# Performance work log

Measured on AMD Instinct MI355X. Metric: run time of the kernel, lower is better.

The kernel has to match this reference:

```python
import jax, jax.numpy as jnp
import numpy as np

N, NCLS, D = 512, 100000, 128
SCALE, MARGIN = 64.0, 0.5
EPS_BN = 1e-5
EPS_NORM = 1e-12


def _init_conv(key, shape):
    # Kaiming-ish init for conv weights (OIHW)
    fan_in = float(np.prod(shape[1:]))
    return jax.random.normal(key, shape, jnp.float32) * np.float32(np.sqrt(2.0 / fan_in))


def setup_inputs() -> dict:
    key = jax.random.key(0)
    ks = jax.random.split(key, 8)
    return {
        "x": jax.random.normal(ks[0], (N, 1, 112, 112), jnp.float32),
        "gt": jax.random.randint(ks[1], (N,), 0, NCLS, dtype=jnp.int32),
        "w1": _init_conv(ks[2], (16, 1, 4, 4)),  "b1": jnp.zeros(16),  "g1": jnp.ones(16),  "be1": jnp.zeros(16),
        "w2": _init_conv(ks[3], (32, 16, 4, 4)), "b2": jnp.zeros(32),  "g2": jnp.ones(32),  "be2": jnp.zeros(32),
        "w3": _init_conv(ks[4], (64, 32, 3, 3)), "b3": jnp.zeros(64),  "g3": jnp.ones(64),  "be3": jnp.zeros(64),
        "w4": _init_conv(ks[5], (128, 64, 3, 3)),"b4": jnp.zeros(128), "g4": jnp.ones(128), "be4": jnp.zeros(128),
        # xavier-uniform ArcFace weight (out_size, in_size)
        "arc_w": jax.random.uniform(ks[6], (NCLS, D), jnp.float32, -1.0, 1.0) * np.float32(np.sqrt(6.0 / (NCLS + D))),
    }


def _conv_bn_relu(x, w, b, g, be, stride, pad):
    y = jax.lax.conv_general_dilated(
        x, w, (stride, stride), [(pad, pad), (pad, pad)],
        dimension_numbers=("NCHW", "OIHW", "NCHW"))
    y = y + b[None, :, None, None]
    # BatchNorm in training mode: batch statistics, biased variance
    mu = y.mean((0, 2, 3), keepdims=True)
    var = ((y - mu) ** 2).mean((0, 2, 3), keepdims=True)
    yn = (y - mu) * jax.lax.rsqrt(var + EPS_BN)
    return jax.nn.relu(yn * g[None, :, None, None] + be[None, :, None, None])


def _l2norm(v):
    return v / jnp.maximum(jnp.linalg.norm(v, axis=1, keepdims=True), EPS_NORM)


def reference(x, gt, w1, b1, g1, be1, w2, b2, g2, be2, w3, b3, g3, be3,
              w4, b4, g4, be4, arc_w):
    h = _conv_bn_relu(x, w1, b1, g1, be1, stride=2, pad=1)   # (N,16,56,56)
    h = _conv_bn_relu(h, w2, b2, g2, be2, stride=2, pad=1)   # (N,32,28,28)
    h = _conv_bn_relu(h, w3, b3, g3, be3, stride=1, pad=0)   # (N,64,26,26)
    h = _conv_bn_relu(h, w4, b4, g4, be4, stride=1, pad=0)   # (N,128,24,24)
    f = h.mean((2, 3))                                        # global avg pool -> (N,128)

    logit = _l2norm(f) @ _l2norm(arc_w).T                     # (N, NCLS) cosine logits
    n = logit.shape[0]
    rows = jnp.arange(n)
    orig = logit[rows, gt]                                    # target cosines
    marg = jnp.cos(jnp.arccos(orig) + MARGIN)                 # cos(theta + m)
    out = logit.at[rows, gt].add(marg - orig)                 # scatter margin correction
    return SCALE * out
```

## Files before the change

kernel.cpp:

```cpp
#include <hip/hip_runtime.h>

typedef unsigned int uint;
typedef unsigned short ushort;

typedef _Float16 half8 __attribute__((ext_vector_type(8)));
typedef float f32x4 __attribute__((ext_vector_type(4)));

#define DEV __device__ __forceinline__

DEV ushort f2h(float x) {
    _Float16 h = (_Float16)x;
    ushort u;
    __builtin_memcpy(&u, &h, 2);
    return u;
}

__global__ __launch_bounds__(256, 2) void conv1_k(
    const float* __restrict__ x, const float* __restrict__ w,
    const float* __restrict__ bias, ushort* __restrict__ y1,
    float* __restrict__ sums)
{
    int idx = blockIdx.x * 256 + threadIdx.x;
    int ow = idx % 56;
    int oh = (idx / 56) % 56;
    int n  = idx / 3136;

    float acc[16];
#pragma unroll
    for (int o = 0; o < 16; ++o) acc[o] = bias[o];

    const float* xp = x + (size_t)n * 12544;
#pragma unroll
    for (int kh = 0; kh < 4; ++kh) {
        int ih = oh * 2 - 1 + kh;
        if ((uint)ih >= 112u) continue;
#pragma unroll
        for (int kw = 0; kw < 4; ++kw) {
            int iw = ow * 2 - 1 + kw;
            if ((uint)iw >= 112u) continue;
            float v = xp[ih * 112 + iw];
#pragma unroll
            for (int o = 0; o < 16; ++o)
                acc[o] = fmaf(v, w[o * 16 + kh * 4 + kw], acc[o]);
        }
    }

    ushort hs[16];
#pragma unroll
    for (int o = 0; o < 16; ++o) hs[o] = f2h(acc[o]);
    __builtin_memcpy(y1 + (size_t)idx * 16, hs, 32);

    __shared__ float red[2][4][16];
    int lane = threadIdx.x & 63, wv = threadIdx.x >> 6;
#pragma unroll
    for (int o = 0; o < 16; ++o) {
        float s = acc[o], q = acc[o] * acc[o];
#pragma unroll
        for (int off = 32; off; off >>= 1) {
            s += __shfl_down(s, off);
            q += __shfl_down(q, off);
        }
        if (lane == 0) { red[0][wv][o] = s; red[1][wv][o] = q; }
    }
    __syncthreads();
    float* sl = sums + (blockIdx.x & 7) * 256;
    int t = threadIdx.x;
    if (t < 16)
        atomicAdd(&sl[t], red[0][0][t] + red[0][1][t] + red[0][2][t] + red[0][3][t]);
    else if (t >= 64 && t < 80) {
        int o = t - 64;
        atomicAdd(&sl[128 + o], red[1][0][o] + red[1][1][o] + red[1][2][o] + red[1][3][o]);
    }
}

__global__ __launch_bounds__(128) void mkab(const float* __restrict__ sums,
                                            const float* __restrict__ g,
                                            const float* __restrict__ be,
                                            float* __restrict__ ab, int C, float invP)
{
    int c = threadIdx.x;
    if (c >= C) return;
    float s = 0.f, q = 0.f;
#pragma unroll
    for (int k = 0; k < 8; ++k) { s += sums[k * 256 + c]; q += sums[k * 256 + 128 + c]; }
    float mu  = s * invP;
    float var = fmaf(-mu, mu, q * invP);
    float a   = g[c] / sqrtf(var + 1e-5f);
    ab[c]     = a;
    ab[C + c] = fmaf(-mu, a, be[c]);
}

template <int C>
__global__ __launch_bounds__(256) void fold(const ushort* __restrict__ y,
                                            const float* __restrict__ ab,
                                            ushort* __restrict__ h)
{
    __shared__ float sa[C], sb[C];
    if (threadIdx.x < C) { sa[threadIdx.x] = ab[threadIdx.x]; sb[threadIdx.x] = ab[C + threadIdx.x]; }
    __syncthreads();
    int idx = blockIdx.x * 256 + threadIdx.x;
    half8 v;
    __builtin_memcpy(&v, y + (size_t)idx * 8, 16);
    int c0 = (idx * 8) & (C - 1);
    half8 o;
#pragma unroll
    for (int e = 0; e < 8; ++e) {
        float f = (float)v[e];
        o[e] = (_Float16)fmaxf(fmaf(sa[c0 + e], f, sb[c0 + e]), 0.f);
    }
    __builtin_memcpy(h + (size_t)idx * 8, &o, 16);
}

template <int OC, int IC, int K>
__global__ __launch_bounds__(256) void repack(const float* __restrict__ w,
                                              ushort* __restrict__ wb)
{
    int i = blockIdx.x * 256 + threadIdx.x;
    int ic = i % IC;
    int r  = i / IC;
    int kw = r % K;  r /= K;
    int kh = r % K;
    int oc = r / K;
    wb[i] = f2h(w[((oc * IC + ic) * K + kh) * K + kw]);
}

template <int OC, int IC, int K>
__global__ __launch_bounds__(256) void repack_cm(const float* __restrict__ w,
                                                 ushort* __restrict__ wb)
{
    constexpr int NC = IC / 32;
    int i = blockIdx.x * 256 + threadIdx.x;
    int e  = i & 31;
    int oc = (i >> 5) % OC;
    int q  = i / (32 * OC);
    int c  = q % NC;
    int r  = q / NC;
    int kw = r % K, kh = r / K;
    int ic = c * 32 + e;
    wb[i] = f2h(w[((oc * IC + ic) * K + kh) * K + kw]);
}

__global__ __launch_bounds__(256, 2) void conv2_mfma(
    const ushort* __restrict__ hin, const ushort* __restrict__ wb,
    const float* __restrict__ bias, ushort* __restrict__ y,
    float* __restrict__ sums)
{
    const int lane = threadIdx.x & 63, wv = threadIdx.x >> 6;
    const int col = lane & 15, quad = lane >> 4;
    const int kwoff = quad >> 1;
    const int icoff = (quad & 1) * 8;
    const int mbase = blockIdx.x * 128 + wv * 32;

    int nb[2], ihb[2], iwb[2];
#pragma unroll
    for (int s = 0; s < 2; ++s) {
        int m = mbase + s * 16 + col;
        int n = m / 784, rem = m % 784;
        int oh = rem / 28, ow = rem % 28;
        nb[s]  = n * 50176 + icoff;
        ihb[s] = oh * 2 - 1;
        iwb[s] = ow * 2 - 1 + kwoff;
    }

    float bv[2];
#pragma unroll
    for (int t = 0; t < 2; ++t) bv[t] = bias[t * 16 + col];

    f32x4 acc[2][2];
#pragma unroll
    for (int s = 0; s < 2; ++s)
#pragma unroll
        for (int t = 0; t < 2; ++t) acc[s][t] = (f32x4){0.f, 0.f, 0.f, 0.f};

    const int wrow = col * 256 + icoff;

#pragma unroll
    for (int kh = 0; kh < 4; ++kh) {
#pragma unroll
        for (int kwp = 0; kwp < 2; ++kwp) {
            half8 af[2];
#pragma unroll
            for (int s = 0; s < 2; ++s) {
                int ih = ihb[s] + kh;
                int iw = iwb[s] + kwp * 2;
                uint r0 = 0, r1 = 0, r2 = 0, r3 = 0;
                if ((uint)ih < 56u && (uint)iw < 56u) {
                    uint raw[4];
                    __builtin_memcpy(raw, hin + nb[s] + ih * 896 + iw * 16, 16);
                    r0 = raw[0]; r1 = raw[1]; r2 = raw[2]; r3 = raw[3];
                }
                uint raw2[4] = {r0, r1, r2, r3};
                __builtin_memcpy(&af[s], raw2, 16);
            }
            const int boff = (kh * 4 + kwp * 2 + kwoff) * 16;
#pragma unroll
            for (int t = 0; t < 2; ++t) {
                half8 bf;
                __builtin_memcpy(&bf, wb + wrow + t * 4096 + boff, 16);
#pragma unroll
                for (int s = 0; s < 2; ++s)
                    acc[s][t] = __builtin_amdgcn_mfma_f32_16x16x32_f16(af[s], bf, acc[s][t], 0, 0, 0);
            }
        }
    }

    float ss[2] = {0.f, 0.f}, qq[2] = {0.f, 0.f};
#pragma unroll
    for (int s = 0; s < 2; ++s) {
        int m0 = mbase + s * 16 + quad * 4;
#pragma unroll
        for (int t = 0; t < 2; ++t) {
#pragma unroll
            for (int r = 0; r < 4; ++r) {
                float yv = acc[s][t][r] + bv[t];
                ss[t] += yv;
                qq[t] = fmaf(yv, yv, qq[t]);
                y[(size_t)(m0 + r) * 32 + t * 16 + col] = f2h(yv);
            }
        }
    }
    __shared__ float redS[4][32], redQ[4][32];
#pragma unroll
    for (int t = 0; t < 2; ++t) {
        float s = ss[t], q = qq[t];
        s += __shfl_xor(s, 16); s += __shfl_xor(s, 32);
        q += __shfl_xor(q, 16); q += __shfl_xor(q, 32);
        if (quad == 0) { redS[wv][t * 16 + col] = s; redQ[wv][t * 16 + col] = q; }
    }
    __syncthreads();
    int t0 = threadIdx.x;
    float* sl = sums + (blockIdx.x & 7) * 256;
    if (t0 < 32)
        atomicAdd(&sl[t0], redS[0][t0] + redS[1][t0] + redS[2][t0] + redS[3][t0]);
    else if (t0 >= 128 && t0 < 160) {
        int c = t0 - 128;
        atomicAdd(&sl[128 + c], redQ[0][c] + redQ[1][c] + redQ[2][c] + redQ[3][c]);
    }
}

template <int IC, int OC, int K, int IH, int IW, int OH, int OW>
__global__ __launch_bounds__(256, 2) void conv_lds(
    const ushort* __restrict__ hin, const ushort* __restrict__ wb,
    const float* __restrict__ bias, ushort* __restrict__ y,
    float* __restrict__ sums)
{
    constexpr int NT  = OC / 16, NC = IC / 32;
    constexpr int NCH = K * K * NC;
    constexpr int ROWB = IW * IC * 2;
    constexpr int MAXR = 255 / OW + K;
    constexpr int SLAB = ((MAXR * ROWB + 4095) / 4096) * 4096;
    __shared__ ushort slab[SLAB / 2];
    __shared__ float redS[4][OC], redQ[4][OC];

    const int lane = threadIdx.x & 63, wv = threadIdx.x >> 6;
    const int col = lane & 15, quad = lane >> 4;
    const int mbase = blockIdx.x * 256 + wv * 64;

    const int m0  = blockIdx.x * 256;
    const int rl0 = (m0 / (OH * OW)) * IH + (m0 % (OH * OW)) / OW;
    const int mL  = m0 + 255;
    const int rl1 = (mL / (OH * OW)) * IH + (mL % (OH * OW)) / OW + (K - 1);
    const int stage_bytes = (rl1 - rl0 + 1) * ROWB;

    {
        const char* src = (const char*)(hin + (size_t)rl0 * (IW * IC));
        char* dst = (char*)slab;
        int d = threadIdx.x * 16;
        int rounds = (stage_bytes + 4095) >> 12;
        for (int r = 0; r < rounds; ++r) {
            int sw = d ^ (((d >> 7) & 7) << 4);
            __builtin_amdgcn_global_load_lds(
                (const __attribute__((address_space(1))) void*)(src + sw),
                (__attribute__((address_space(3))) void*)(dst + d), 16, 0, 0);
            d += 4096;
        }
    }

    int aloc[4];
#pragma unroll
    for (int s = 0; s < 4; ++s) {
        int m = mbase + s * 16 + col;
        int n = m / (OH * OW), rem = m % (OH * OW);
        int oh = rem / OW, ow = rem % OW;
        aloc[s] = ((n * IH + oh - rl0) * IW + ow) * IC + quad * 8;
    }
    const int bcol = col * 32 + quad * 8;

    f32x4 acc[4][NT];
#pragma unroll
    for (int s = 0; s < 4; ++s)
#pragma unroll
        for (int t = 0; t < NT; ++t) acc[s][t] = (f32x4){0.f, 0.f, 0.f, 0.f};

    half8 bbuf[2][NT];
#pragma unroll
    for (int t = 0; t < NT; ++t)
        __builtin_memcpy(&bbuf[0][t], wb + t * 512 + bcol, 16);

    __syncthreads();

#pragma unroll
    for (int q = 0; q < NCH; ++q) {
        if (q + 1 < NCH) {
            const ushort* bp = wb + (q + 1) * (OC * 32) + bcol;
#pragma unroll
            for (int t = 0; t < NT; ++t)
                __builtin_memcpy(&bbuf[(q + 1) & 1][t], bp + t * 512, 16);
        }
        const int kh = q / (K * NC), kw = (q / NC) % K, c = q % NC;
        const int aoff = (kh * IW + kw) * IC + c * 32;
#pragma unroll
        for (int s = 0; s < 4; ++s) {
            half8 af;
            int b = 2 * (aloc[s] + aoff);
            b ^= ((b >> 7) & 7) << 4;
            __builtin_memcpy(&af, (const char*)slab + b, 16);
#pragma unroll
            for (int t = 0; t < NT; ++t)
                acc[s][t] = __builtin_amdgcn_mfma_f32_16x16x32_f16(af, bbuf[q & 1][t], acc[s][t], 0, 0, 0);
        }
    }

    float bv[NT];
#pragma unroll
    for (int t = 0; t < NT; ++t) bv[t] = bias[t * 16 + col];

    float ss[NT], qq[NT];
#pragma unroll
    for (int t = 0; t < NT; ++t) { ss[t] = 0.f; qq[t] = 0.f; }
#pragma unroll
    for (int s = 0; s < 4; ++s) {
        int me = mbase + s * 16 + quad * 4;
#pragma unroll
        for (int t = 0; t < NT; ++t) {
#pragma unroll
            for (int r = 0; r < 4; ++r) {
                float yv = acc[s][t][r] + bv[t];
                ss[t] += yv;
                qq[t] = fmaf(yv, yv, qq[t]);
                y[(size_t)(me + r) * OC + t * 16 + col] = f2h(yv);
            }
        }
    }
#pragma unroll
    for (int t = 0; t < NT; ++t) {
        float s = ss[t], q = qq[t];
        s += __shfl_xor(s, 16); s += __shfl_xor(s, 32);
        q += __shfl_xor(q, 16); q += __shfl_xor(q, 32);
        if (quad == 0) { redS[wv][t * 16 + col] = s; redQ[wv][t * 16 + col] = q; }
    }
    __syncthreads();
    int t0 = threadIdx.x;
    float* sl = sums + (blockIdx.x & 7) * 256;
    if (t0 < OC)
        atomicAdd(&sl[t0], redS[0][t0] + redS[1][t0] + redS[2][t0] + redS[3][t0]);
    else if (t0 >= 128 && t0 < 128 + OC) {
        int c = t0 - 128;
        atomicAdd(&sl[128 + c], redQ[0][c] + redQ[1][c] + redQ[2][c] + redQ[3][c]);
    }
}

__global__ __launch_bounds__(256) void pool(const ushort* __restrict__ y4,
                                            const float* __restrict__ ab,
                                            float* __restrict__ f)
{
    int n = blockIdx.x;
    int c = threadIdx.x & 127, ph = threadIdx.x >> 7;
    const ushort* p = y4 + (size_t)n * 73728 + c;
    float a = ab[c], b = ab[128 + c];
    float s = 0.f;
    for (int i = ph * 288; i < ph * 288 + 288; ++i) {
        _Float16 hv;
        __builtin_memcpy(&hv, p + i * 128, 2);
        s += fmaxf(fmaf(a, (float)hv, b), 0.f);
    }
    __shared__ float l[128];
    if (ph == 1) l[c] = s;
    __syncthreads();
    if (ph == 0) f[n * 128 + c] = (s + l[c]) * (1.f / 576.f);
}

__global__ __launch_bounds__(128) void fnorm(const float* __restrict__ f,
                                             ushort* __restrict__ fnh)
{
    int n = blockIdx.x, t = threadIdx.x;
    float v = f[n * 128 + t];
    float q = v * v;
    for (int off = 32; off; off >>= 1) q += __shfl_down(q, off);
    __shared__ float l[2];
    if ((t & 63) == 0) l[t >> 6] = q;
    __syncthreads();
    float inv = 1.f / fmaxf(sqrtf(l[0] + l[1]), 1e-12f);
    fnh[n * 128 + t] = f2h(v * inv);
}

__global__ __launch_bounds__(256) void wpack(const float* __restrict__ w,
                                             ushort* __restrict__ w16)
{
    int wv = threadIdx.x >> 6, lane = threadIdx.x & 63;
    int j = blockIdx.x * 4 + wv;
    const float* p = w + (size_t)j * 128;
    float v0 = p[lane], v1 = p[lane + 64];
    float q = fmaf(v0, v0, v1 * v1);
#pragma unroll
    for (int off = 32; off; off >>= 1) q += __shfl_down(q, off);
    float inv = 1.f / fmaxf(sqrtf(__shfl(q, 0)), 1e-12f);
    w16[(size_t)j * 128 + lane]      = f2h(v0 * inv);
    w16[(size_t)j * 128 + lane + 64] = f2h(v1 * inv);
}

__global__ __launch_bounds__(256) void arc_gemm(const ushort* __restrict__ fnh,
                                                const ushort* __restrict__ w16,
                                                const int* __restrict__ gt,
                                                float* __restrict__ out)
{
    const int lane = threadIdx.x & 63, wv = threadIdx.x >> 6;
    const int col = lane & 15, quad = lane >> 4;
    const int jbase = blockIdx.x * 64 + wv * 16;
    if (jbase >= 100000) return;

    half8 bfr[4];
    const ushort* wp = w16 + (size_t)(jbase + col) * 128 + quad * 8;
#pragma unroll
    for (int s = 0; s < 4; ++s)
        __builtin_memcpy(&bfr[s], wp + s * 32, 16);

    const float cm = 0.87758256189037272f;
    const float sm = 0.47942553860420301f;
    const int j0 = jbase + quad * 4;

    half8 afA[4], afB[4];
    const ushort* ap0 = fnh + (size_t)col * 128 + quad * 8;
#pragma unroll
    for (int s = 0; s < 4; ++s)
        __builtin_memcpy(&afA[s], ap0 + s * 32, 16);

    auto step = [&](int mt, half8 (&cur)[4], half8 (&nxt)[4]) {
        if (mt + 1 < 32) {
            const ushort* apn = fnh + (size_t)((mt + 1) * 16 + col) * 128 + quad * 8;
#pragma unroll
            for (int s = 0; s < 4; ++s)
                __builtin_memcpy(&nxt[s], apn + s * 32, 16);
        }
        f32x4 acc = {0.f, 0.f, 0.f, 0.f};
#pragma unroll
        for (int s = 0; s < 4; ++s)
            acc = __builtin_amdgcn_mfma_f32_16x16x32_f16(bfr[s], cur[s], acc, 0, 0, 0);

        const int m = mt * 16 + col;
        const int d = gt[m] - j0;
        if ((uint)d < 4u) {
#pragma unroll
            for (int r = 0; r < 4; ++r)
                if (r == d) {
                    float v = acc[r];
                    float t = fmaxf(1.f - v * v, 0.f);
                    acc[r] = fmaf(v, cm, -sqrtf(t) * sm);
                }
        }
        f32x4 o4;
#pragma unroll
        for (int r = 0; r < 4; ++r) o4[r] = 64.f * acc[r];
        __builtin_nontemporal_store(o4, (f32x4*)(out + (size_t)m * 100000 + j0));
    };

    for (int mt = 0; mt < 32; mt += 2) {
        step(mt, afA, afB);
        step(mt + 1, afB, afA);
    }
}

extern "C" void kernel_launch(void* const* d_in, const int* in_sizes, int n_in,
                              void* d_out, int out_size, void* d_ws, size_t ws_size,
                              hipStream_t stream)
{
    const float* x   = (const float*)d_in[0];
    const int*   gt  = (const int*)d_in[1];
    const float* w1  = (const float*)d_in[2];
    const float* b1  = (const float*)d_in[3];
    const float* g1  = (const float*)d_in[4];
    const float* be1 = (const float*)d_in[5];
    const float* w2  = (const float*)d_in[6];
    const float* b2  = (const float*)d_in[7];
    const float* g2  = (const float*)d_in[8];
    const float* be2 = (const float*)d_in[9];
    const float* w3  = (const float*)d_in[10];
    const float* b3  = (const float*)d_in[11];
    const float* g3  = (const float*)d_in[12];
    const float* be3 = (const float*)d_in[13];
    const float* w4  = (const float*)d_in[14];
    const float* b4  = (const float*)d_in[15];
    const float* g4  = (const float*)d_in[16];
    const float* be4 = (const float*)d_in[17];
    const float* aw  = (const float*)d_in[18];
    float* out = (float*)d_out;

    float* ws = (float*)d_ws;
    ushort* yb  = (ushort*)ws;
    ushort* hb  = (ushort*)(ws + 18874368);
    ushort* w16 = hb;
    ushort* wb2 = (ushort*)(ws + 31719424);
    ushort* wb3 = (ushort*)(ws + 31723520);
    ushort* wb4 = (ushort*)(ws + 31732736);
    float* sums = ws + 31769600;
    float* ab   = ws + 31777792;
    float* fbuf = ws + 31778816;
    ushort* fnh = (ushort*)(ws + 31844352);

    hipMemsetAsync(sums, 0, 4 * 2048 * sizeof(float), stream);

    repack<32, 16, 4><<<32, 256, 0, stream>>>(w2, wb2);
    repack_cm<64, 32, 3><<<72, 256, 0, stream>>>(w3, wb3);
    repack_cm<128, 64, 3><<<288, 256, 0, stream>>>(w4, wb4);

    conv1_k<<<6272, 256, 0, stream>>>(x, w1, b1, yb, sums);
    mkab<<<1, 128, 0, stream>>>(sums, g1, be1, ab, 16, 1.f / 1605632.f);
    fold<16><<<12544, 256, 0, stream>>>(yb, ab, hb);

    conv2_mfma<<<3136, 256, 0, stream>>>(hb, wb2, b2, yb, sums + 2048);
    mkab<<<1, 128, 0, stream>>>(sums + 2048, g2, be2, ab + 256, 32, 1.f / 401408.f);
    fold<32><<<6272, 256, 0, stream>>>(yb, ab + 256, hb);

    conv_lds<32, 64, 3, 28, 28, 26, 26><<<1352, 256, 0, stream>>>(hb, wb3, b3, yb, sums + 4096);
    mkab<<<1, 128, 0, stream>>>(sums + 4096, g3, be3, ab + 512, 64, 1.f / 346112.f);
    fold<64><<<10816, 256, 0, stream>>>(yb, ab + 512, hb);

    conv_lds<64, 128, 3, 26, 26, 24, 24><<<1152, 256, 0, stream>>>(hb, wb4, b4, yb, sums + 6144);
    mkab<<<1, 128, 0, stream>>>(sums + 6144, g4, be4, ab + 768, 128, 1.f / 294912.f);

    wpack<<<25000, 256, 0, stream>>>(aw, w16);

    pool<<<512, 256, 0, stream>>>(yb, ab + 768, fbuf);
    fnorm<<<512, 128, 0, stream>>>(fbuf, fnh);

    arc_gemm<<<1563, 256, 0, stream>>>(fnh, w16, gt, out);
}
```

Measured before the change: 634.5 us.

## Stage conv2 input in LDS, vectorize pool, widen ArcFace GEMM tiles

conv2 now copies the needed input rows into shared memory with asynchronous global-to-LDS loads and a swizzled layout. Each block computes 256 output positions, weights are repacked for contiguous fragment loads, and the next weight fragment is prefetched while the current one is used. The pool kernel reads eight channels per 16-byte load and reduces partial sums through shared memory. The ArcFace GEMM makes each wave cover two 16-column tiles, so activation fragments are reused and the grid is halved. These changes trade more LDS and registers per block for lower occupancy.

```diff
diff --git a/kernel.cpp b/kernel.cpp
--- a/kernel.cpp
+++ b/kernel.cpp
@@ -111,17 +111,17 @@
     __builtin_memcpy(h + (size_t)idx * 8, &o, 16);
 }
 
-template <int OC, int IC, int K>
-__global__ __launch_bounds__(256) void repack(const float* __restrict__ w,
-                                              ushort* __restrict__ wb)
+__global__ __launch_bounds__(256) void repack_c2(const float* __restrict__ w,
+                                                 ushort* __restrict__ wb)
 {
     int i = blockIdx.x * 256 + threadIdx.x;
-    int ic = i % IC;
-    int r  = i / IC;
-    int kw = r % K;  r /= K;
-    int kh = r % K;
-    int oc = r / K;
-    wb[i] = f2h(w[((oc * IC + ic) * K + kh) * K + kw]);
+    int e  = i & 31;
+    int oc = (i >> 5) & 31;
+    int q  = i >> 10;
+    int kh = q >> 1, kwp = q & 1;
+    int kw = kwp * 2 + (e >> 4);
+    int ic = e & 15;
+    wb[i] = f2h(w[((oc * 16 + ic) * 4 + kh) * 4 + kw]);
 }
 
 template <int OC, int IC, int K>
@@ -140,74 +140,104 @@
     wb[i] = f2h(w[((oc * IC + ic) * K + kh) * K + kw]);
 }
 
-__global__ __launch_bounds__(256, 2) void conv2_mfma(
+__global__ __launch_bounds__(256, 2) void conv2_lds(
     const ushort* __restrict__ hin, const ushort* __restrict__ wb,
     const float* __restrict__ bias, ushort* __restrict__ y,
     float* __restrict__ sums)
 {
+    constexpr int ROWB = 56 * 16 * 2;
+    constexpr int SLAB = ((24 * ROWB + 4095) / 4096) * 4096;
+    __shared__ ushort slab[SLAB / 2];
+    __shared__ float redS[4][32], redQ[4][32];
+
     const int lane = threadIdx.x & 63, wv = threadIdx.x >> 6;
     const int col = lane & 15, quad = lane >> 4;
     const int kwoff = quad >> 1;
     const int icoff = (quad & 1) * 8;
-    const int mbase = blockIdx.x * 128 + wv * 32;
-
-    int nb[2], ihb[2], iwb[2];
-#pragma unroll
-    for (int s = 0; s < 2; ++s) {
+    const int mbase = blockIdx.x * 256 + wv * 64;
+
+    const int m0 = blockIdx.x * 256;
+    const int r0 = m0 / 28;
+    const int rL = (m0 + 255) / 28;
+    const int rl0 = max(2 * r0 - 1, 0);
+    const int rl1 = min(2 * rL + 2, 512 * 56 - 1);
+    const int stage_bytes = (rl1 - rl0 + 1) * ROWB;
+
+    {
+        const char* src = (const char*)(hin + (size_t)rl0 * 896);
+        char* dst = (char*)slab;
+        int d = threadIdx.x * 16;
+        int rounds = (stage_bytes + 4095) >> 12;
+        for (int r = 0; r < rounds; ++r) {
+            int sw = d ^ (((d >> 7) & 7) << 4);
+            __builtin_amdgcn_global_load_lds(
+                (const __attribute__((address_space(1))) void*)(src + sw),
+                (__attribute__((address_space(3))) void*)(dst + d), 16, 0, 0);
+            d += 4096;
+        }
+    }
+
+    int nbase[4], ihb[4], iwb[4];
+#pragma unroll
+    for (int s = 0; s < 4; ++s) {
         int m = mbase + s * 16 + col;
         int n = m / 784, rem = m % 784;
         int oh = rem / 28, ow = rem % 28;
-        nb[s]  = n * 50176 + icoff;
+        nbase[s] = n * 56 - rl0;
         ihb[s] = oh * 2 - 1;
         iwb[s] = ow * 2 - 1 + kwoff;
     }
+    const int bcol = col * 32 + quad * 8;
+
+    f32x4 acc[4][2];
+#pragma unroll
+    for (int s = 0; s < 4; ++s)
+#pragma unroll
+        for (int t = 0; t < 2; ++t) acc[s][t] = (f32x4){0.f, 0.f, 0.f, 0.f};
+
+    half8 bbuf[2][2];
+#pragma unroll
+    for (int t = 0; t < 2; ++t)
+        __builtin_memcpy(&bbuf[0][t], wb + t * 512 + bcol, 16);
+
+    __syncthreads();
+
+#pragma unroll
+    for (int q = 0; q < 8; ++q) {
+        if (q + 1 < 8) {
+            const ushort* bp = wb + (q + 1) * 1024 + bcol;
+#pragma unroll
+            for (int t = 0; t < 2; ++t)
+                __builtin_memcpy(&bbuf[(q + 1) & 1][t], bp + t * 512, 16);
+        }
+        const int kh = q >> 1, kwp = q & 1;
+#pragma unroll
+        for (int s = 0; s < 4; ++s) {
+            int ih = ihb[s] + kh;
+            int iw = iwb[s] + kwp * 2;
+            bool valid = ((uint)ih < 56u) && ((uint)iw < 56u);
+            int off = valid ? ((nbase[s] + ih) * 896 + iw * 16 + icoff) : 0;
+            int b = 2 * off;
+            b ^= ((b >> 7) & 7) << 4;
+            uint raw[4];
+            __builtin_memcpy(raw, (const char*)slab + b, 16);
+            if (!valid) { raw[0] = 0; raw[1] = 0; raw[2] = 0; raw[3] = 0; }
+            half8 af;
+            __builtin_memcpy(&af, raw, 16);
+#pragma unroll
+            for (int t = 0; t < 2; ++t)
+                acc[s][t] = __builtin_amdgcn_mfma_f32_16x16x32_f16(af, bbuf[q & 1][t], acc[s][t], 0, 0, 0);
+        }
+    }
 
     float bv[2];
 #pragma unroll
     for (int t = 0; t < 2; ++t) bv[t] = bias[t * 16 + col];
 
-    f32x4 acc[2][2];
-#pragma unroll
-    for (int s = 0; s < 2; ++s)
-#pragma unroll
-        for (int t = 0; t < 2; ++t) acc[s][t] = (f32x4){0.f, 0.f, 0.f, 0.f};
-
-    const int wrow = col * 256 + icoff;
-
-#pragma unroll
-    for (int kh = 0; kh < 4; ++kh) {
-#pragma unroll
-        for (int kwp = 0; kwp < 2; ++kwp) {
-            half8 af[2];
-#pragma unroll
-            for (int s = 0; s < 2; ++s) {
-                int ih = ihb[s] + kh;
-                int iw = iwb[s] + kwp * 2;
-                uint r0 = 0, r1 = 0, r2 = 0, r3 = 0;
-                if ((uint)ih < 56u && (uint)iw < 56u) {
-                    uint raw[4];
-                    __builtin_memcpy(raw, hin + nb[s] + ih * 896 + iw * 16, 16);
-                    r0 = raw[0]; r1 = raw[1]; r2 = raw[2]; r3 = raw[3];
-                }
-                uint raw2[4] = {r0, r1, r2, r3};
-                __builtin_memcpy(&af[s], raw2, 16);
-            }
-            const int boff = (kh * 4 + kwp * 2 + kwoff) * 16;
-#pragma unroll
-            for (int t = 0; t < 2; ++t) {
-                half8 bf;
-                __builtin_memcpy(&bf, wb + wrow + t * 4096 + boff, 16);
-#pragma unroll
-                for (int s = 0; s < 2; ++s)
-                    acc[s][t] = __builtin_amdgcn_mfma_f32_16x16x32_f16(af[s], bf, acc[s][t], 0, 0, 0);
-            }
-        }
-    }
-
     float ss[2] = {0.f, 0.f}, qq[2] = {0.f, 0.f};
 #pragma unroll
-    for (int s = 0; s < 2; ++s) {
-        int m0 = mbase + s * 16 + quad * 4;
+    for (int s = 0; s < 4; ++s) {
+        int me = mbase + s * 16 + quad * 4;
 #pragma unroll
         for (int t = 0; t < 2; ++t) {
 #pragma unroll
@@ -215,11 +245,10 @@
                 float yv = acc[s][t][r] + bv[t];
                 ss[t] += yv;
                 qq[t] = fmaf(yv, yv, qq[t]);
-                y[(size_t)(m0 + r) * 32 + t * 16 + col] = f2h(yv);
+                y[(size_t)(me + r) * 32 + t * 16 + col] = f2h(yv);
             }
         }
     }
-    __shared__ float redS[4][32], redQ[4][32];
 #pragma unroll
     for (int t = 0; t < 2; ++t) {
         float s = ss[t], q = qq[t];
@@ -365,19 +394,32 @@
                                             float* __restrict__ f)
 {
     int n = blockIdx.x;
-    int c = threadIdx.x & 127, ph = threadIdx.x >> 7;
-    const ushort* p = y4 + (size_t)n * 73728 + c;
-    float a = ab[c], b = ab[128 + c];
-    float s = 0.f;
-    for (int i = ph * 288; i < ph * 288 + 288; ++i) {
-        _Float16 hv;
-        __builtin_memcpy(&hv, p + i * 128, 2);
-        s += fmaxf(fmaf(a, (float)hv, b), 0.f);
-    }
-    __shared__ float l[128];
-    if (ph == 1) l[c] = s;
-    __syncthreads();
-    if (ph == 0) f[n * 128 + c] = (s + l[c]) * (1.f / 576.f);
+    int g = threadIdx.x & 15, ph = threadIdx.x >> 4;
+    const ushort* p = y4 + (size_t)n * 73728 + g * 8;
+    float a8[8], b8[8];
+#pragma unroll
+    for (int e = 0; e < 8; ++e) { a8[e] = ab[g * 8 + e]; b8[e] = ab[128 + g * 8 + e]; }
+    float s8[8];
+#pragma unroll
+    for (int e = 0; e < 8; ++e) s8[e] = 0.f;
+    for (int i = ph; i < 576; i += 16) {
+        half8 v;
+        __builtin_memcpy(&v, p + i * 128, 16);
+#pragma unroll
+        for (int e = 0; e < 8; ++e)
+            s8[e] += fmaxf(fmaf(a8[e], (float)v[e], b8[e]), 0.f);
+    }
+    __shared__ float l[16][128];
+#pragma unroll
+    for (int e = 0; e < 8; ++e) l[ph][g * 8 + e] = s8[e];
+    __syncthreads();
+    if (threadIdx.x < 128) {
+        int c = threadIdx.x;
+        float s = 0.f;
+#pragma unroll
+        for (int k = 0; k < 16; ++k) s += l[k][c];
+        f[n * 128 + c] = s * (1.f / 576.f);
+    }
 }
 
 __global__ __launch_bounds__(128) void fnorm(const float* __restrict__ f,
@@ -416,18 +458,20 @@
 {
     const int lane = threadIdx.x & 63, wv = threadIdx.x >> 6;
     const int col = lane & 15, quad = lane >> 4;
-    const int jbase = blockIdx.x * 64 + wv * 16;
+    const int jbase = blockIdx.x * 128 + wv * 32;
     if (jbase >= 100000) return;
 
-    half8 bfr[4];
-    const ushort* wp = w16 + (size_t)(jbase + col) * 128 + quad * 8;
-#pragma unroll
-    for (int s = 0; s < 4; ++s)
-        __builtin_memcpy(&bfr[s], wp + s * 32, 16);
+    half8 bfr[2][4];
+#pragma unroll
+    for (int jt = 0; jt < 2; ++jt) {
+        const ushort* wp = w16 + (size_t)(jbase + jt * 16 + col) * 128 + quad * 8;
+#pragma unroll
+        for (int s = 0; s < 4; ++s)
+            __builtin_memcpy(&bfr[jt][s], wp + s * 32, 16);
+    }
 
     const float cm = 0.87758256189037272f;
     const float sm = 0.47942553860420301f;
-    const int j0 = jbase + quad * 4;
 
     half8 afA[4], afB[4];
     const ushort* ap0 = fnh + (size_t)col * 128 + quad * 8;
@@ -442,26 +486,34 @@
             for (int s = 0; s < 4; ++s)
                 __builtin_memcpy(&nxt[s], apn + s * 32, 16);
         }
-        f32x4 acc = {0.f, 0.f, 0.f, 0.f};
-#pragma unroll
-        for (int s = 0; s < 4; ++s)
-            acc = __builtin_amdgcn_mfma_f32_16x16x32_f16(bfr[s], cur[s], acc, 0, 0, 0);
-
+        f32x4 acc0 = {0.f, 0.f, 0.f, 0.f};
+        f32x4 acc1 = {0.f, 0.f, 0.f, 0.f};
+#pragma unroll
+        for (int s = 0; s < 4; ++s) {
+            acc0 = __builtin_amdgcn_mfma_f32_16x16x32_f16(bfr[0][s], cur[s], acc0, 0, 0, 0);
+            acc1 = __builtin_amdgcn_mfma_f32_16x16x32_f16(bfr[1][s], cur[s], acc1, 0, 0, 0);
+        }
         const int m = mt * 16 + col;
-        const int d = gt[m] - j0;
-        if ((uint)d < 4u) {
-#pragma unroll
-            for (int r = 0; r < 4; ++r)
-                if (r == d) {
-                    float v = acc[r];
-                    float t = fmaxf(1.f - v * v, 0.f);
-                    acc[r] = fmaf(v, cm, -sqrtf(t) * sm);
-                }
-        }
-        f32x4 o4;
-#pragma unroll
-        for (int r = 0; r < 4; ++r) o4[r] = 64.f * acc[r];
-        __builtin_nontemporal_store(o4, (f32x4*)(out + (size_t)m * 100000 + j0));
+        const int g = gt[m];
+#pragma unroll
+        for (int jt = 0; jt < 2; ++jt) {
+            f32x4& acc = jt ? acc1 : acc0;
+            const int j0 = jbase + jt * 16 + quad * 4;
+            const int d = g - j0;
+            if ((uint)d < 4u) {
+#pragma unroll
+                for (int r = 0; r < 4; ++r)
+                    if (r == d) {
+                        float v = acc[r];
+                        float t = fmaxf(1.f - v * v, 0.f);
+                        acc[r] = fmaf(v, cm, -sqrtf(t) * sm);
+                    }
+            }
+            f32x4 o4;
+#pragma unroll
+            for (int r = 0; r < 4; ++r) o4[r] = 64.f * acc[r];
+            __builtin_nontemporal_store(o4, (f32x4*)(out + (size_t)m * 100000 + j0));
+        }
     };
 
     for (int mt = 0; mt < 32; mt += 2) {
@@ -509,7 +561,7 @@
 
     hipMemsetAsync(sums, 0, 4 * 2048 * sizeof(float), stream);
 
-    repack<32, 16, 4><<<32, 256, 0, stream>>>(w2, wb2);
+    repack_c2<<<32, 256, 0, stream>>>(w2, wb2);
     repack_cm<64, 32, 3><<<72, 256, 0, stream>>>(w3, wb3);
     repack_cm<128, 64, 3><<<288, 256, 0, stream>>>(w4, wb4);
 
@@ -517,7 +569,7 @@
     mkab<<<1, 128, 0, stream>>>(sums, g1, be1, ab, 16, 1.f / 1605632.f);
     fold<16><<<12544, 256, 0, stream>>>(yb, ab, hb);
 
-    conv2_mfma<<<3136, 256, 0, stream>>>(hb, wb2, b2, yb, sums + 2048);
+    conv2_lds<<<1568, 256, 0, stream>>>(hb, wb2, b2, yb, sums + 2048);
     mkab<<<1, 128, 0, stream>>>(sums + 2048, g2, be2, ab + 256, 32, 1.f / 401408.f);
     fold<32><<<6272, 256, 0, stream>>>(yb, ab + 256, hb);
 
@@ -533,5 +585,5 @@
     pool<<<512, 256, 0, stream>>>(yb, ab + 768, fbuf);
     fnorm<<<512, 128, 0, stream>>>(fbuf, fnh);
 
-    arc_gemm<<<1563, 256, 0, stream>>>(fnh, w16, gt, out);
-}
+    arc_gemm<<<782, 256, 0, stream>>>(fnh, w16, gt, out);
+}
```

Result: faster. 588.1 us (-7.3%).
